# Optimization experiments

Hardware: AMD Instinct MI355X
Metric: run time of the kernel (lower is better)

Reference implementation:

```python
import jax, jax.numpy as jnp
import numpy as np

N, MAX_DEG, F_IN, F_OUT = 20000, 32, 128, 128
TRIM_RATIO = 0.45
N_NEIGH_THRESHOLD = 3


def setup_inputs() -> dict:
    key = jax.random.key(0)
    k_h, k_nbr, k_deg, k_w, k_b = jax.random.split(key, 5)
    h = jax.random.normal(k_h, (N, F_IN), dtype=jnp.float32)
    nbr = jax.random.randint(k_nbr, (N, MAX_DEG), 0, N, dtype=jnp.int32)
    # in-degree in [1, MAX_DEG] so every node has at least one neighbor
    deg = jax.random.randint(k_deg, (N,), 1, MAX_DEG + 1, dtype=jnp.int32)
    # GCN symmetric normalizer deg^-0.5, per node, shape [N, 1]
    norm = (deg.astype(jnp.float32) ** -0.5)[:, None]
    stdv = 1.0 / np.sqrt(F_OUT)
    weight = jax.random.uniform(k_w, (F_IN, F_OUT), jnp.float32, -stdv, stdv)
    bias = jax.random.uniform(k_b, (F_OUT,), jnp.float32, -stdv, stdv)
    return {"h": h, "norm": norm, "weight": weight, "bias": bias,
            "nbr": nbr, "deg": deg}


def reference(h, norm, weight, bias, nbr, deg):
    # h: [N,F] node features (dropout=0 so input_ft == dropped_h == h)
    # nbr: [N,D] padded src indices; deg: [N] valid neighbor counts; norm: [N,1]
    D = nbr.shape[1]
    slot = jnp.arange(D, dtype=deg.dtype)[None, :]            # [1,D]
    valid = slot < deg[:, None]                                # [N,D]

    h_nbr = h[nbr]                                             # [N,D,F] = mailbox input_ft
    msg = h_nbr * norm[nbr]                                    # [N,D,F] = mailbox m (src h * src norm)

    # padded slots -> +inf so they sort past all valid entries (ranks >= deg)
    big = jnp.asarray(jnp.finfo(h.dtype).max, h.dtype)
    ift = jnp.where(valid[..., None], h_nbr, big)
    sidx = jnp.argsort(ift, axis=1)                            # per-feature sort over neighbors
    gathered = jnp.take_along_axis(msg, sidx, axis=1)          # [N,D,F]

    n = deg                                                    # per-node n_neigh
    b_raw = n // 2 - (1 - n % 2)
    b_cap = jnp.floor(n.astype(jnp.float32) * TRIM_RATIO).astype(n.dtype)
    b = jnp.maximum(jnp.minimum(b_raw, b_cap), 1)              # trim count per node

    # keep sorted ranks in [b, n-b)
    sel = (slot >= b[:, None]) & (slot < (n - b)[:, None])     # [N,D]
    trimmed_sum = jnp.sum(gathered * sel[..., None].astype(h.dtype), axis=1)  # [N,F]

    self0 = h * norm                                           # dst h * dst norm (mailbox 'self'[:,0])
    alpha = (2 * b).astype(h.dtype)[:, None]
    accum_med = (trimmed_sum + self0 * alpha) * norm           # trim_compensate=True branch
    accum_small = (n.astype(h.dtype)[:, None] * self0) * norm  # n_neigh <= threshold branch
    accum = jnp.where((n <= N_NEIGH_THRESHOLD)[:, None], accum_small, accum_med)

    # NodeApplyModule_V2: linear + bias + relu
    out = jax.nn.relu(accum @ weight + bias)
    return out
```

## Files before the change

kernel.cpp:

```cpp
#include <hip/hip_runtime.h>
#include <hip/hip_fp16.h>
#include <cfloat>
#include <cmath>

#define N_NODES 20000
#define MAXD 32
#define F 128

#define MTILE 64
#define NBLK ((N_NODES + MTILE - 1) / MTILE)
#define MPAD (NBLK * MTILE)
#define WT_PITCH 136

typedef _Float16 half8 __attribute__((ext_vector_type(8)));
typedef float f32x4 __attribute__((ext_vector_type(4)));


template <int SZ, int NV>
__device__ __forceinline__ void oe_sort_n(float (&a)[SZ]) {
#pragma unroll
  for (int p = 1; p < SZ; p <<= 1) {
#pragma unroll
    for (int q = p; q >= 1; q >>= 1) {
#pragma unroll
      for (int j = q % p; j <= SZ - 1 - q; j += 2 * q) {
#pragma unroll
        for (int i = 0; i < q; ++i) {
          int x = i + j, y = i + j + q;
          if (y < NV && (x / (2 * p)) == (y / (2 * p))) {
            float mn = fminf(a[x], a[y]);
            float mx = fmaxf(a[x], a[y]);
            a[x] = mn;
            a[y] = mx;
          }
        }
      }
    }
  }
}

template <int N>
struct TrimB {
  static constexpr int b_raw = N / 2 - (1 - (N & 1));
  static constexpr int b_cap = (int)((float)N * 0.45f);
  static constexpr int b_min = b_raw < b_cap ? b_raw : b_cap;
  static constexpr int value = b_min > 1 ? b_min : 1;
};

template <int SZ, int N>
__device__ __forceinline__ float trimmed_sum_n(const float* __restrict__ h,
                                               const float* __restrict__ norm,
                                               const int* __restrict__ nbr_row,
                                               int f) {
  constexpr int B = TrimB<N>::value;
  constexpr int NB = N - B;

  float ko[SZ];
  float nrm[SZ];
  float k[SZ];
#pragma unroll
  for (int d = 0; d < N; ++d) {
    int src = nbr_row[d];
    nrm[d] = norm[src];
    ko[d] = h[src * F + f];
    k[d] = ko[d];
  }
#pragma unroll
  for (int d = N; d < SZ; ++d) k[d] = FLT_MAX;

  oe_sort_n<SZ, N>(k);

  const float lo  = k[B];
  const float hi  = k[NB - 1];
  const float lom = k[B - 1];
  const float him = k[NB];

  float sum = 0.f;
  if ((lom < lo) & (hi < him)) {
#pragma unroll
    for (int d = 0; d < N; ++d) {
      bool keep = (ko[d] >= lo) & (ko[d] <= hi);
      sum = fmaf(keep ? ko[d] : 0.f, nrm[d], sum);
    }
  } else {
    int c_lt_lo = 0, c_lt_hi = 0;
#pragma unroll
    for (int d = 0; d < N; ++d) {
      c_lt_lo += (ko[d] < lo) ? 1 : 0;
      c_lt_hi += (ko[d] < hi) ? 1 : 0;
    }
    int run_lo = 0, run_hi = 0;
#pragma unroll
    for (int d = 0; d < N; ++d) {
      const float kd = ko[d];
      const float m = kd * nrm[d];
      const bool eql = (kd == lo);
      const bool eqh = (kd == hi);
      const bool lh = (lo < hi);
      const bool btw = (kd > lo) & (kd < hi);
      const int r_lo = c_lt_lo + run_lo;
      const int r_hi = c_lt_hi + run_hi;
      const bool inc = btw
                     | (eql & (r_lo >= B) & (lh | (r_lo < NB)))
                     | (lh & eqh & (r_hi < NB));
      sum += inc ? m : 0.f;
      run_lo += eql ? 1 : 0;
      run_hi += eqh ? 1 : 0;
    }
  }
  return sum;
}

__device__ __forceinline__ void store_split(_Float16* __restrict__ Ah,
                                            _Float16* __restrict__ Al,
                                            int idx, float v) {
  _Float16 hi = (_Float16)v;
  Ah[idx] = hi;
  Al[idx] = (_Float16)(v - (float)hi);
}

__global__ __launch_bounds__(128) void gcn_stage1(const float* __restrict__ h,
                                                  const float* __restrict__ norm,
                                                  const int* __restrict__ nbr,
                                                  const int* __restrict__ deg,
                                                  _Float16* __restrict__ Ah,
                                                  _Float16* __restrict__ Al) {
  const int i = blockIdx.x;
  const int f = threadIdx.x;
  const int n = deg[i];
  const float ni = norm[i];
  const float hif = h[i * F + f];
  const int idx = i * F + f;

  if (n <= 3) {
    store_split(Ah, Al, idx, (float)n * hif * ni * ni);
    return;
  }

  const int* nbr_row = nbr + i * MAXD;
  float ts;
  int b;
  switch (n) {
#define TS_CASE(NN, SS) \
    case NN: ts = trimmed_sum_n<SS, NN>(h, norm, nbr_row, f); b = TrimB<NN>::value; break;
    TS_CASE(4, 4)
    TS_CASE(5, 8) TS_CASE(6, 8) TS_CASE(7, 8) TS_CASE(8, 8)
    TS_CASE(9, 16) TS_CASE(10, 16) TS_CASE(11, 16) TS_CASE(12, 16)
    TS_CASE(13, 16) TS_CASE(14, 16) TS_CASE(15, 16) TS_CASE(16, 16)
    TS_CASE(17, 32) TS_CASE(18, 32) TS_CASE(19, 32) TS_CASE(20, 32)
    TS_CASE(21, 32) TS_CASE(22, 32) TS_CASE(23, 32) TS_CASE(24, 32)
    TS_CASE(25, 32) TS_CASE(26, 32) TS_CASE(27, 32) TS_CASE(28, 32)
    TS_CASE(29, 32) TS_CASE(30, 32) TS_CASE(31, 32)
    default: ts = trimmed_sum_n<32, 32>(h, norm, nbr_row, f); b = TrimB<32>::value; break;
#undef TS_CASE
  }

  store_split(Ah, Al, idx, (ts + hif * ni * (float)(2 * b)) * ni);
}

__global__ __launch_bounds__(256) void gcn_gemm_mfma(
    const _Float16* __restrict__ Ah, const _Float16* __restrict__ Al,
    const float* __restrict__ W, const float* __restrict__ bias,
    float* __restrict__ out) {
  __shared__ _Float16 Wt[2][F][WT_PITCH];
  const int t = threadIdx.x;

#pragma unroll 4
  for (int i = 0; i < 64; ++i) {
    int idx = i * 256 + t;
    int k = idx >> 7, n = idx & 127;
    float w = W[idx];
    _Float16 hi = (_Float16)w;
    Wt[0][n][k] = hi;
    Wt[1][n][k] = (_Float16)(w - (float)hi);
  }
  __syncthreads();

  const int lane = t & 63;
  const int wv = t >> 6;
  const int l16 = lane & 15;
  const int kg = lane >> 4;
  const int row0 = blockIdx.x * MTILE;
  const int colb = wv * 32;

  f32x4 acc[4][2];
#pragma unroll
  for (int rf = 0; rf < 4; ++rf)
#pragma unroll
    for (int cf = 0; cf < 2; ++cf) acc[rf][cf] = (f32x4){0.f, 0.f, 0.f, 0.f};

#pragma unroll
  for (int kc = 0; kc < F; kc += 32) {
    half8 ah[4], al[4], bh[2], bl[2];
#pragma unroll
    for (int rf = 0; rf < 4; ++rf) {
      const int row = row0 + rf * 16 + l16;
      const size_t off = (size_t)row * F + kc + kg * 8;
      ah[rf] = *(const half8*)(Ah + off);
      al[rf] = *(const half8*)(Al + off);
    }
#pragma unroll
    for (int cf = 0; cf < 2; ++cf) {
      const int n = colb + cf * 16 + l16;
      bh[cf] = *(const half8*)(&Wt[0][n][kc + kg * 8]);
      bl[cf] = *(const half8*)(&Wt[1][n][kc + kg * 8]);
    }
#pragma unroll
    for (int rf = 0; rf < 4; ++rf)
#pragma unroll
      for (int cf = 0; cf < 2; ++cf) {
        acc[rf][cf] = __builtin_amdgcn_mfma_f32_16x16x32_f16(ah[rf], bh[cf], acc[rf][cf], 0, 0, 0);
        acc[rf][cf] = __builtin_amdgcn_mfma_f32_16x16x32_f16(ah[rf], bl[cf], acc[rf][cf], 0, 0, 0);
        acc[rf][cf] = __builtin_amdgcn_mfma_f32_16x16x32_f16(al[rf], bh[cf], acc[rf][cf], 0, 0, 0);
      }
  }

#pragma unroll
  for (int cf = 0; cf < 2; ++cf) {
    const int col = colb + cf * 16 + l16;
    const float bv = bias[col];
#pragma unroll
    for (int rf = 0; rf < 4; ++rf) {
#pragma unroll
      for (int r = 0; r < 4; ++r) {
        const int row = row0 + rf * 16 + kg * 4 + r;
        if (row < N_NODES) {
          out[(size_t)row * F + col] = fmaxf(acc[rf][cf][r] + bv, 0.f);
        }
      }
    }
  }
}

extern "C" void kernel_launch(void* const* d_in, const int* in_sizes, int n_in,
                              void* d_out, int out_size, void* d_ws, size_t ws_size,
                              hipStream_t stream) {
  const float* h = (const float*)d_in[0];
  const float* norm = (const float*)d_in[1];
  const float* weight = (const float*)d_in[2];
  const float* bias = (const float*)d_in[3];
  const int* nbr = (const int*)d_in[4];
  const int* deg = (const int*)d_in[5];
  float* out = (float*)d_out;

  _Float16* Ah = (_Float16*)d_ws;
  _Float16* Al = Ah + (size_t)MPAD * F;

  gcn_stage1<<<N_NODES, 128, 0, stream>>>(h, norm, nbr, deg, Ah, Al);
  gcn_gemm_mfma<<<NBLK, 256, 0, stream>>>(Ah, Al, weight, bias, out);
}
```

Baseline: 116.4 us.

## Pre-split weights in stage1, pack hi/lo activations, shrink GEMM tile

The first 16 blocks of the aggregation kernel now split the weight matrix into transposed fp16 hi/lo halves and write them to workspace. The GEMM reads these from global memory, so it no longer converts W into shared memory in every block. Activations are stored as packed hi/lo pairs in one 32-bit word, written with a single store and split apart with vector shuffles. The GEMM tile drops from 64 to 32 rows, doubling the block count for better occupancy on a small GEMM, and the row bound check is removed. The risk is that the hot W fragments now come from L2/global instead of LDS.

```diff
diff --git a/kernel.cpp b/kernel.cpp
--- a/kernel.cpp
+++ b/kernel.cpp
@@ -7,13 +7,13 @@
 #define MAXD 32
 #define F 128
 
-#define MTILE 64
-#define NBLK ((N_NODES + MTILE - 1) / MTILE)
-#define MPAD (NBLK * MTILE)
-#define WT_PITCH 136
+#define MTILE 32
+#define NBLK (N_NODES / MTILE)
 
 typedef _Float16 half8 __attribute__((ext_vector_type(8)));
 typedef float f32x4 __attribute__((ext_vector_type(4)));
+typedef unsigned int u32x4 __attribute__((ext_vector_type(4)));
+typedef unsigned short us8v __attribute__((ext_vector_type(8)));
 
 
 template <int SZ, int NV>
@@ -111,29 +111,44 @@
   return sum;
 }
 
-__device__ __forceinline__ void store_split(_Float16* __restrict__ Ah,
-                                            _Float16* __restrict__ Al,
-                                            int idx, float v) {
+__device__ __forceinline__ unsigned int split_pack(float v) {
   _Float16 hi = (_Float16)v;
-  Ah[idx] = hi;
-  Al[idx] = (_Float16)(v - (float)hi);
+  _Float16 lo = (_Float16)(v - (float)hi);
+  unsigned short hb = __builtin_bit_cast(unsigned short, hi);
+  unsigned short lb = __builtin_bit_cast(unsigned short, lo);
+  return (unsigned int)hb | ((unsigned int)lb << 16);
 }
 
 __global__ __launch_bounds__(128) void gcn_stage1(const float* __restrict__ h,
                                                   const float* __restrict__ norm,
                                                   const int* __restrict__ nbr,
                                                   const int* __restrict__ deg,
-                                                  _Float16* __restrict__ Ah,
-                                                  _Float16* __restrict__ Al) {
+                                                  const float* __restrict__ W,
+                                                  unsigned int* __restrict__ Ap,
+                                                  _Float16* __restrict__ Whl) {
   const int i = blockIdx.x;
   const int f = threadIdx.x;
+
+  if (i < 16) {
+    const int e0 = (i * 128 + f) * 8;
+#pragma unroll
+    for (int j = 0; j < 8; ++j) {
+      const int e = e0 + j;
+      const int k = e >> 7, n = e & 127;
+      const float w = W[e];
+      const _Float16 whi = (_Float16)w;
+      Whl[n * F + k] = whi;
+      Whl[16384 + n * F + k] = (_Float16)(w - (float)whi);
+    }
+  }
+
   const int n = deg[i];
   const float ni = norm[i];
   const float hif = h[i * F + f];
   const int idx = i * F + f;
 
   if (n <= 3) {
-    store_split(Ah, Al, idx, (float)n * hif * ni * ni);
+    Ap[idx] = split_pack((float)n * hif * ni * ni);
     return;
   }
 
@@ -155,27 +170,13 @@
 #undef TS_CASE
   }
 
-  store_split(Ah, Al, idx, (ts + hif * ni * (float)(2 * b)) * ni);
+  Ap[idx] = split_pack((ts + hif * ni * (float)(2 * b)) * ni);
 }
 
 __global__ __launch_bounds__(256) void gcn_gemm_mfma(
-    const _Float16* __restrict__ Ah, const _Float16* __restrict__ Al,
-    const float* __restrict__ W, const float* __restrict__ bias,
-    float* __restrict__ out) {
-  __shared__ _Float16 Wt[2][F][WT_PITCH];
+    const unsigned int* __restrict__ Ap, const _Float16* __restrict__ Whl,
+    const float* __restrict__ bias, float* __restrict__ out) {
   const int t = threadIdx.x;
-
-#pragma unroll 4
-  for (int i = 0; i < 64; ++i) {
-    int idx = i * 256 + t;
-    int k = idx >> 7, n = idx & 127;
-    float w = W[idx];
-    _Float16 hi = (_Float16)w;
-    Wt[0][n][k] = hi;
-    Wt[1][n][k] = (_Float16)(w - (float)hi);
-  }
-  __syncthreads();
-
   const int lane = t & 63;
   const int wv = t >> 6;
   const int l16 = lane & 15;
@@ -183,30 +184,36 @@
   const int row0 = blockIdx.x * MTILE;
   const int colb = wv * 32;
 
-  f32x4 acc[4][2];
-#pragma unroll
-  for (int rf = 0; rf < 4; ++rf)
+  f32x4 acc[2][2];
+#pragma unroll
+  for (int rf = 0; rf < 2; ++rf)
 #pragma unroll
     for (int cf = 0; cf < 2; ++cf) acc[rf][cf] = (f32x4){0.f, 0.f, 0.f, 0.f};
 
 #pragma unroll
   for (int kc = 0; kc < F; kc += 32) {
-    half8 ah[4], al[4], bh[2], bl[2];
-#pragma unroll
-    for (int rf = 0; rf < 4; ++rf) {
+    half8 ah[2], al[2], bh[2], bl[2];
+#pragma unroll
+    for (int rf = 0; rf < 2; ++rf) {
       const int row = row0 + rf * 16 + l16;
-      const size_t off = (size_t)row * F + kc + kg * 8;
-      ah[rf] = *(const half8*)(Ah + off);
-      al[rf] = *(const half8*)(Al + off);
+      const unsigned int* p = Ap + (size_t)row * F + kc + kg * 8;
+      u32x4 p0 = *(const u32x4*)p;
+      u32x4 p1 = *(const u32x4*)(p + 4);
+      us8v s0 = __builtin_bit_cast(us8v, p0);
+      us8v s1 = __builtin_bit_cast(us8v, p1);
+      ah[rf] = __builtin_bit_cast(half8,
+          (us8v)__builtin_shufflevector(s0, s1, 0, 2, 4, 6, 8, 10, 12, 14));
+      al[rf] = __builtin_bit_cast(half8,
+          (us8v)__builtin_shufflevector(s0, s1, 1, 3, 5, 7, 9, 11, 13, 15));
     }
 #pragma unroll
     for (int cf = 0; cf < 2; ++cf) {
       const int n = colb + cf * 16 + l16;
-      bh[cf] = *(const half8*)(&Wt[0][n][kc + kg * 8]);
-      bl[cf] = *(const half8*)(&Wt[1][n][kc + kg * 8]);
-    }
-#pragma unroll
-    for (int rf = 0; rf < 4; ++rf)
+      bh[cf] = *(const half8*)(Whl + n * F + kc + kg * 8);
+      bl[cf] = *(const half8*)(Whl + 16384 + n * F + kc + kg * 8);
+    }
+#pragma unroll
+    for (int rf = 0; rf < 2; ++rf)
 #pragma unroll
       for (int cf = 0; cf < 2; ++cf) {
         acc[rf][cf] = __builtin_amdgcn_mfma_f32_16x16x32_f16(ah[rf], bh[cf], acc[rf][cf], 0, 0, 0);
@@ -220,13 +227,11 @@
     const int col = colb + cf * 16 + l16;
     const float bv = bias[col];
 #pragma unroll
-    for (int rf = 0; rf < 4; ++rf) {
+    for (int rf = 0; rf < 2; ++rf) {
 #pragma unroll
       for (int r = 0; r < 4; ++r) {
         const int row = row0 + rf * 16 + kg * 4 + r;
-        if (row < N_NODES) {
-          out[(size_t)row * F + col] = fmaxf(acc[rf][cf][r] + bv, 0.f);
-        }
+        out[(size_t)row * F + col] = fmaxf(acc[rf][cf][r] + bv, 0.f);
       }
     }
   }
@@ -243,9 +248,9 @@
   const int* deg = (const int*)d_in[5];
   float* out = (float*)d_out;
 
-  _Float16* Ah = (_Float16*)d_ws;
-  _Float16* Al = Ah + (size_t)MPAD * F;
-
-  gcn_stage1<<<N_NODES, 128, 0, stream>>>(h, norm, nbr, deg, Ah, Al);
-  gcn_gemm_mfma<<<NBLK, 256, 0, stream>>>(Ah, Al, weight, bias, out);
-}
+  unsigned int* Ap = (unsigned int*)d_ws;
+  _Float16* Whl = (_Float16*)(Ap + (size_t)N_NODES * F);
+
+  gcn_stage1<<<N_NODES, 128, 0, stream>>>(h, norm, nbr, deg, weight, Ap, Whl);
+  gcn_gemm_mfma<<<NBLK, 256, 0, stream>>>(Ap, Whl, bias, out);
+}
```

Result: faster. 112.7 us (median of 2 runs) (-3.1%).
